# Optimization experiments

Hardware: AMD Instinct MI355X
Metric: run time of the kernel (lower is better)

Reference implementation:

```python
import jax, jax.numpy as jnp
import numpy as np

EMB = 64   # embedding_dim
OUT = 64   # out_channels (== EMB so conv layers stack)
EF = 16    # num_edge_features
L = 2      # num_layers
NC, NT = 5000, 10000
E, EL = 50000, 20000


def setup_inputs():
    key = jax.random.key(0)
    it = iter(jax.random.split(key, 40))
    def nrm(shape, s=0.05):
        return jax.random.normal(next(it), shape, dtype=jnp.float32) * s
    def ri(n, hi):
        return jax.random.randint(next(it), (n,), 0, hi, dtype=jnp.int32)
    return dict(
        x_c=jnp.arange(NC, dtype=jnp.int32),
        x_t=jnp.arange(NT, dtype=jnp.int32),
        edge_src_ct=ri(E, NC), edge_dst_ct=ri(E, NT),
        edge_src_tc=ri(E, NT), edge_dst_tc=ri(E, NC),
        edge_label_src=ri(EL, NC), edge_label_dst=ri(EL, NT),
        edge_attr_ct=nrm((E, EF), 1.0),
        edge_attr_tc=nrm((E, EF), 1.0),
        edge_label_attr=nrm((EL, EF), 1.0),
        emb_c=nrm((NC, EMB), 1.0), emb_t=nrm((NT, EMB), 1.0),
        ntl_c_w=nrm((EMB, EMB)), ntl_c_b=nrm((EMB,)),
        ntl_t_w=nrm((EMB, EMB)), ntl_t_b=nrm((EMB,)),
        conv_mlp1_w=nrm((L, 2, EF, OUT)), conv_mlp1_b=nrm((L, 2, OUT)),
        conv_mlp2_w=nrm((L, 2, OUT, EMB * OUT)), conv_mlp2_b=nrm((L, 2, EMB * OUT)),
        conv_root_w=nrm((L, 2, EMB, OUT)), conv_root_b=nrm((L, 2, OUT)),
        ph_w0=nrm((2 * EMB + EF, 64)), ph_b0=nrm((64,)),
        ph_w1=nrm((64, 64)), ph_b1=nrm((64,)),
        ph_w2=nrm((64, 1)), ph_b2=nrm((1,)),
    )


def _nnconv(h_src, h_dst, src, dst, eattr, m1w, m1b, m2w, m2b, rw, rb, n_dst):
    # edge-conditioned weight matrices: [E, EMB, OUT]
    W = (jax.nn.relu(eattr @ m1w + m1b) @ m2w + m2b).reshape(-1, EMB, OUT)
    msg = jnp.einsum('ei,eio->eo', h_src[src], W)        # gather + per-edge matmul
    agg = jax.ops.segment_max(msg, dst, num_segments=n_dst)
    agg = jnp.where(jnp.isneginf(agg), 0.0, agg)         # isolated nodes -> 0 (PyG semantics)
    return agg + h_dst @ rw + rb                          # root weight + bias


def reference(x_c, x_t, edge_src_ct, edge_dst_ct, edge_src_tc, edge_dst_tc,
              edge_label_src, edge_label_dst, edge_attr_ct, edge_attr_tc,
              edge_label_attr, emb_c, emb_t, ntl_c_w, ntl_c_b, ntl_t_w, ntl_t_b,
              conv_mlp1_w, conv_mlp1_b, conv_mlp2_w, conv_mlp2_b,
              conv_root_w, conv_root_b, ph_w0, ph_b0, ph_w1, ph_b1, ph_w2, ph_b2):
    h_c = emb_c[x_c] @ ntl_c_w + ntl_c_b
    h_t = emb_t[x_t] @ ntl_t_w + ntl_t_b
    for l in range(L):
        new_t = _nnconv(h_c, h_t, edge_src_ct, edge_dst_ct, edge_attr_ct,
                        conv_mlp1_w[l, 0], conv_mlp1_b[l, 0], conv_mlp2_w[l, 0],
                        conv_mlp2_b[l, 0], conv_root_w[l, 0], conv_root_b[l, 0], NT)
        new_c = _nnconv(h_t, h_c, edge_src_tc, edge_dst_tc, edge_attr_tc,
                        conv_mlp1_w[l, 1], conv_mlp1_b[l, 1], conv_mlp2_w[l, 1],
                        conv_mlp2_b[l, 1], conv_root_w[l, 1], conv_root_b[l, 1], NC)
        h_c, h_t = jax.nn.relu(new_c), jax.nn.relu(new_t)
    z = jnp.concatenate([h_c[edge_label_src], h_t[edge_label_dst], edge_label_attr], axis=-1)
    z = jax.nn.relu(z @ ph_w0 + ph_b0)
    z = jax.nn.relu(z @ ph_w1 + ph_b1)
    logits = z @ ph_w2 + ph_b2
    preds = jax.nn.sigmoid(logits).squeeze()
    return preds, logits
```

## Files before the change

kernel.cpp:

```cpp
#include <hip/hip_runtime.h>
#include <hip/hip_bf16.h>
#include <math.h>

#define NCN   5000
#define NTN   10000
#define NEDGE 50000
#define NLBL  20000
#define EPB   448
#define EBLK  112
#define ESLOT 50176
#define MT    7

typedef _Float16 f16x8 __attribute__((ext_vector_type(8)));
typedef _Float16 f16x4 __attribute__((ext_vector_type(4)));
typedef float    f32x4 __attribute__((ext_vector_type(4)));

#define HSTRIDE 456
#define NSLICE  130
#define ZSTR    72

__device__ __forceinline__ void stage16(const _Float16* g, _Float16* l) {
  __builtin_amdgcn_global_load_lds(
      (const __attribute__((address_space(1))) void*)g,
      (__attribute__((address_space(3))) void*)l, 16, 0, 0);
}

__global__ __launch_bounds__(256) void prep_B(
    const float* __restrict__ m2w, const float* __restrict__ m2b,
    _Float16* __restrict__ out)
{
  int p = blockIdx.x / NSLICE;
  int s = blockIdx.x % NSLICE;
  int t = threadIdx.x;
  int hi = t >> 6, col = t & 63;
  const float* w  = m2w + p * 64 * 4096;
  const float* bb = m2b + p * 4096;
  f16x8 v;
  #pragma unroll
  for (int j = 0; j < 8; ++j) {
    float x;
    if (s < 128) {
      int h = s >> 1, i = (s & 1) * 32 + hi * 8 + j;
      x = w[h * 4096 + i * 64 + col];
    } else {
      int i = (s - 128) * 32 + hi * 8 + j;
      x = bb[i * 64 + col];
    }
    v[j] = (_Float16)x;
  }
  *(f16x8*)(out + ((size_t)(p * NSLICE + s)) * 2048 + t * 8) = v;
}

__global__ __launch_bounds__(256) void prep_m1(
    const float* __restrict__ m1w, const float* __restrict__ m1b,
    _Float16* __restrict__ out)
{
  int p = blockIdx.x;
  int t = threadIdx.x;
  int hi = t >> 6, col = t & 63;
  f16x8 v;
  #pragma unroll
  for (int j = 0; j < 8; ++j) {
    int i = hi * 8 + j;
    float x = (i < 16) ? m1w[p * 1024 + i * 64 + col]
            : (i == 16) ? m1b[p * 64 + col] : 0.0f;
    v[j] = (_Float16)x;
  }
  *(f16x8*)(out + (size_t)p * 2048 + t * 8) = v;
}

__global__ __launch_bounds__(256) void prep_headB(
    const float* __restrict__ w0, const float* __restrict__ b0,
    const float* __restrict__ w1, const float* __restrict__ b1,
    _Float16* __restrict__ out)
{
  int s = blockIdx.x;
  int t = threadIdx.x;
  int hi = t >> 6, col = t & 63;
  f16x8 v;
  #pragma unroll
  for (int j = 0; j < 8; ++j) {
    int k = hi * 8 + j;
    float x = 0.0f;
    if (s < 5) {
      int kr = s * 32 + k;
      x = (kr < 144) ? w0[kr * 64 + col] : (kr == 144 ? b0[col] : 0.0f);
    } else {
      int kr = (s - 5) * 32 + k;
      x = (kr < 64) ? w1[kr * 64 + col] : (kr == 64 ? b1[col] : 0.0f);
    }
    v[j] = (_Float16)x;
  }
  *(f16x8*)(out + (size_t)s * 2048 + t * 8) = v;
}

__global__ __launch_bounds__(256) void count_edges(
    const int* __restrict__ dT, const int* __restrict__ dC,
    int* __restrict__ cT, int* __restrict__ cC)
{
  int i = blockIdx.x * 256 + threadIdx.x;
  if (i < NEDGE) atomicAdd(&cT[dT[i]], 1);
  else { int j = i - NEDGE; if (j < NEDGE) atomicAdd(&cC[dC[j]], 1); }
}

struct ScanArgs { const int* c0; int* o0; int n0; const int* c1; int* o1; int n1; };

__global__ __launch_bounds__(1024) void scan2(ScanArgs a) {
  const int* c = blockIdx.x ? a.c1 : a.c0;
  int*       o = blockIdx.x ? a.o1 : a.o0;
  int        n = blockIdx.x ? a.n1 : a.n0;
  __shared__ int lds[1024];
  int t = threadIdx.x;
  int CH = (n + 1023) / 1024;
  int base = t * CH;
  int s = 0;
  for (int i = 0; i < CH; ++i) { int idx = base + i; if (idx < n) s += c[idx]; }
  lds[t] = s;
  __syncthreads();
  #pragma unroll
  for (int d = 1; d < 1024; d <<= 1) {
    int v = (t >= d) ? lds[t - d] : 0;
    __syncthreads();
    lds[t] += v;
    __syncthreads();
  }
  int run = lds[t] - s;
  for (int i = 0; i < CH; ++i) {
    int idx = base + i;
    if (idx < n) { o[idx] = run; run += c[idx]; }
  }
  if (t == 1023) o[n] = lds[1023];
}

__global__ __launch_bounds__(256) void scatter_edges(
    const int* __restrict__ dT, const int* __restrict__ dC,
    const int* __restrict__ oT, const int* __restrict__ oC,
    int* __restrict__ curT, int* __restrict__ curC,
    int* __restrict__ permT, int* __restrict__ permC)
{
  int i = blockIdx.x * 256 + threadIdx.x;
  if (i < NEDGE) {
    int d = dT[i];
    int p = atomicAdd(&curT[d], 1);
    permT[oT[d] + p] = i;
  } else {
    int j = i - NEDGE;
    if (j < NEDGE) {
      int d = dC[j];
      int p = atomicAdd(&curC[d], 1);
      permC[oC[d] + p] = j;
    }
  }
}

struct NtArgs {
  const float* emb0; const int* idx0; const float* w0; const float* b0; float* out0; int n0; int blk0;
  const float* emb1; const int* idx1; const float* w1; const float* b1; float* out1; int n1;
};

__global__ __launch_bounds__(256) void node_transform2(NtArgs a) {
  int bid = blockIdx.x;
  int dir = (bid >= a.blk0) ? 1 : 0;
  int lb  = bid - (dir ? a.blk0 : 0);
  const float* emb = dir ? a.emb1 : a.emb0;
  const int*   idx = dir ? a.idx1 : a.idx0;
  const float* w   = dir ? a.w1   : a.w0;
  const float* b   = dir ? a.b1   : a.b0;
  float*       out = dir ? a.out1 : a.out0;
  int          n   = dir ? a.n1   : a.n0;

  __shared__ float s_w[64 * 64];
  __shared__ float s_b[64];
  int tid = threadIdx.x;
  for (int i = tid; i < 4096; i += 256) s_w[i] = w[i];
  if (tid < 64) s_b[tid] = b[tid];
  __syncthreads();
  int wave = tid >> 6, lane = tid & 63;
  int node = lb * 4 + wave;
  if (node >= n) return;
  float v = emb[idx[node] * 64 + lane];
  float acc = s_b[lane];
  #pragma unroll 8
  for (int i = 0; i < 64; ++i)
    acc = fmaf(__shfl(v, i, 64), s_w[i * 64 + lane], acc);
  out[node * 64 + lane] = acc;
}

struct ConvArgs {
  const float* h_src0; const int* esrc0; const float* ea0;
  const int* perm0; const _Float16* B0; const _Float16* m10; float* msg0;
  const float* h_src1; const int* esrc1; const float* ea1;
  const int* perm1; const _Float16* B1; const _Float16* m11; float* msg1;
};

__global__ __launch_bounds__(256, 1) void conv_msg_mfma2(ConvArgs a) {
  __shared__ __align__(16) _Float16 s_B[2][4][2048];
  __shared__ __align__(16) _Float16 s_m1f[2048];
  __shared__ __align__(16) _Float16 s_hidT[64 * HSTRIDE];
  __shared__ int s_srcn[EPB];
  __shared__ int s_eidx[EPB];

  const int bid = blockIdx.x;
  const int dir = (bid >= EBLK) ? 1 : 0;
  const int eb  = bid - (dir ? EBLK : 0);

  const float*    h_src  = dir ? a.h_src1 : a.h_src0;
  const int*      esrc   = dir ? a.esrc1  : a.esrc0;
  const float*    eattr  = dir ? a.ea1    : a.ea0;
  const int*      eperm  = dir ? a.perm1  : a.perm0;
  const _Float16* Bready = dir ? a.B1     : a.B0;
  const _Float16* m1rdy  = dir ? a.m11    : a.m10;
  float*          msg    = dir ? a.msg1   : a.msg0;

  const int tid  = threadIdx.x;
  const int e0   = eb * EPB;
  const int w    = tid >> 6;
  const int lane = tid & 63;
  const int l15  = lane & 15;
  const int hi   = lane >> 4;
  const int wE   = w * (MT * 16);

  stage16(m1rdy + tid * 8, &s_m1f[tid * 8]);
  #pragma unroll
  for (int q = 0; q < 4; ++q)
    stage16(Bready + (size_t)q * 2048 + tid * 8, &s_B[0][q][tid * 8]);

  for (int i = tid; i < EPB; i += 256) {
    int e = eperm[e0 + i];
    s_eidx[i] = e;
    s_srcn[i] = esrc[e];
  }
  __syncthreads();

  f16x8 hv0[MT], hv1[MT];
  #pragma unroll
  for (int m = 0; m < MT; ++m) {
    int el = wE + m * 16 + l15;
    const float* src = h_src + (size_t)s_srcn[el] * 64;
    float4 a0 = *(const float4*)(src + hi * 8);
    float4 a1 = *(const float4*)(src + hi * 8 + 4);
    float4 b0 = *(const float4*)(src + 32 + hi * 8);
    float4 b1 = *(const float4*)(src + 32 + hi * 8 + 4);
    hv0[m] = (f16x8){(_Float16)a0.x,(_Float16)a0.y,(_Float16)a0.z,(_Float16)a0.w,
                     (_Float16)a1.x,(_Float16)a1.y,(_Float16)a1.z,(_Float16)a1.w};
    hv1[m] = (f16x8){(_Float16)b0.x,(_Float16)b0.y,(_Float16)b0.z,(_Float16)b0.w,
                     (_Float16)b1.x,(_Float16)b1.y,(_Float16)b1.z,(_Float16)b1.w};
  }

  {
    f16x8 ea[MT];
    #pragma unroll
    for (int m = 0; m < MT; ++m) {
      int li = wE + m * 16 + l15;
      int e  = s_eidx[li];
      f16x8 v = {};
      if (hi < 2) {
        float4 f0 = *(const float4*)(eattr + (size_t)e * 16 + hi * 8);
        float4 f1 = *(const float4*)(eattr + (size_t)e * 16 + hi * 8 + 4);
        v = (f16x8){(_Float16)f0.x,(_Float16)f0.y,(_Float16)f0.z,(_Float16)f0.w,
                    (_Float16)f1.x,(_Float16)f1.y,(_Float16)f1.z,(_Float16)f1.w};
      } else if (hi == 2) {
        v[0] = (_Float16)1.0f;
      }
      ea[m] = v;
    }
    #pragma unroll
    for (int n = 0; n < 4; ++n) {
      f16x8 bm = *(const f16x8*)&s_m1f[(hi * 64 + n * 16 + l15) * 8];
      #pragma unroll
      for (int m = 0; m < MT; ++m) {
        f32x4 hacc = {};
        hacc = __builtin_amdgcn_mfma_f32_16x16x32_f16(ea[m], bm, hacc, 0, 0, 0);
        int h  = n * 16 + l15;
        int e4 = wE + m * 16 + hi * 4;
        f16x4 hval;
        #pragma unroll
        for (int r = 0; r < 4; ++r) hval[r] = (_Float16)fmaxf(hacc[r], 0.0f);
        *(f16x4*)&s_hidT[h * HSTRIDE + e4] = hval;
      }
    }
  }

  f32x4 acc[MT][4] = {};

#define MFMA_SLICE(P_, SS, HV, HH)                                            \
  {                                                                           \
    f16x8 b0 = *(const f16x8*)&s_B[P_][SS][(hi * 64 +  0 + l15) * 8];         \
    f16x8 b1 = *(const f16x8*)&s_B[P_][SS][(hi * 64 + 16 + l15) * 8];         \
    f16x8 b2 = *(const f16x8*)&s_B[P_][SS][(hi * 64 + 32 + l15) * 8];         \
    f16x8 b3 = *(const f16x8*)&s_B[P_][SS][(hi * 64 + 48 + l15) * 8];         \
    _Pragma("unroll")                                                         \
    for (int m = 0; m < MT; ++m) {                                            \
      f16x8 av = (f16x8)(HV[m] * HH[m]);                                      \
      acc[m][0] = __builtin_amdgcn_mfma_f32_16x16x32_f16(av, b0, acc[m][0], 0, 0, 0); \
      acc[m][1] = __builtin_amdgcn_mfma_f32_16x16x32_f16(av, b1, acc[m][1], 0, 0, 0); \
      acc[m][2] = __builtin_amdgcn_mfma_f32_16x16x32_f16(av, b2, acc[m][2], 0, 0, 0); \
      acc[m][3] = __builtin_amdgcn_mfma_f32_16x16x32_f16(av, b3, acc[m][3], 0, 0, 0); \
    }                                                                         \
  }

#define BIAS_SLICE(P_, SS, HV)                                                \
  {                                                                           \
    f16x8 b0 = *(const f16x8*)&s_B[P_][SS][(hi * 64 +  0 + l15) * 8];         \
    f16x8 b1 = *(const f16x8*)&s_B[P_][SS][(hi * 64 + 16 + l15) * 8];         \
    f16x8 b2 = *(const f16x8*)&s_B[P_][SS][(hi * 64 + 32 + l15) * 8];         \
    f16x8 b3 = *(const f16x8*)&s_B[P_][SS][(hi * 64 + 48 + l15) * 8];         \
    _Pragma("unroll")                                                         \
    for (int m = 0; m < MT; ++m) {                                            \
      f16x8 av = HV[m];                                                       \
      acc[m][0] = __builtin_amdgcn_mfma_f32_16x16x32_f16(av, b0, acc[m][0], 0, 0, 0); \
      acc[m][1] = __builtin_amdgcn_mfma_f32_16x16x32_f16(av, b1, acc[m][1], 0, 0, 0); \
      acc[m][2] = __builtin_amdgcn_mfma_f32_16x16x32_f16(av, b2, acc[m][2], 0, 0, 0); \
      acc[m][3] = __builtin_amdgcn_mfma_f32_16x16x32_f16(av, b3, acc[m][3], 0, 0, 0); \
    }                                                                         \
  }

  for (int p = 0; p < 33; ++p) {
    const int P = p & 1;
    if (p < 31) {
      #pragma unroll
      for (int q = 0; q < 4; ++q)
        stage16(Bready + (size_t)(4 * p + 4 + q) * 2048 + tid * 8,
                &s_B[P ^ 1][q][tid * 8]);
    } else if (p == 31) {
      stage16(Bready + (size_t)128 * 2048 + tid * 8, &s_B[P ^ 1][0][tid * 8]);
      stage16(Bready + (size_t)129 * 2048 + tid * 8, &s_B[P ^ 1][1][tid * 8]);
    }
    if (p < 32) {
      _Float16 hA[MT], hB[MT];
      #pragma unroll
      for (int m = 0; m < MT; ++m)
        hA[m] = s_hidT[(2 * p) * HSTRIDE + wE + m * 16 + l15];
      #pragma unroll
      for (int m = 0; m < MT; ++m)
        hB[m] = s_hidT[(2 * p + 1) * HSTRIDE + wE + m * 16 + l15];
      MFMA_SLICE(P, 0, hv0, hA);
      MFMA_SLICE(P, 1, hv1, hA);
      MFMA_SLICE(P, 2, hv0, hB);
      MFMA_SLICE(P, 3, hv1, hB);
    } else {
      BIAS_SLICE(P, 0, hv0);
      BIAS_SLICE(P, 1, hv1);
    }
    asm volatile("s_waitcnt vmcnt(0)" ::: "memory");
    __builtin_amdgcn_s_barrier();
  }
#undef MFMA_SLICE
#undef BIAS_SLICE

  #pragma unroll
  for (int m = 0; m < MT; ++m) {
    #pragma unroll
    for (int r = 0; r < 4; ++r) {
      int sl = e0 + wE + m * 16 + hi * 4 + r;
      float* row = msg + (size_t)sl * 64;
      #pragma unroll
      for (int n = 0; n < 4; ++n)
        row[n * 16 + l15] = acc[m][n][r];
    }
  }
}

struct SegArgs {
  const float* msg0; const int* off0; const float* hold0; const float* rw0; const float* rb0;
  float* hnew0; int n0; int blk0;
  const float* msg1; const int* off1; const float* hold1; const float* rw1; const float* rb1;
  float* hnew1; int n1;
};

__global__ __launch_bounds__(256) void segfin2(SegArgs a) {
  int bid = blockIdx.x;
  int dir = (bid >= a.blk0) ? 1 : 0;
  int lb  = bid - (dir ? a.blk0 : 0);
  const float* msg  = dir ? a.msg1  : a.msg0;
  const int*   off  = dir ? a.off1  : a.off0;
  const float* hold = dir ? a.hold1 : a.hold0;
  const float* rw   = dir ? a.rw1   : a.rw0;
  const float* rb   = dir ? a.rb1   : a.rb0;
  float*       hnew = dir ? a.hnew1 : a.hnew0;
  int          n    = dir ? a.n1    : a.n0;

  __shared__ float s_w[64 * 64];
  __shared__ float s_b[64];
  int tid = threadIdx.x;
  for (int i = tid; i < 4096; i += 256) s_w[i] = rw[i];
  if (tid < 64) s_b[tid] = rb[tid];
  __syncthreads();
  int wave = tid >> 6, lane = tid & 63;
  int node = lb * 4 + wave;
  if (node >= n) return;

  int k0 = off[node], k1 = off[node + 1];
  float mx = -INFINITY;
  for (int k = k0; k < k1; ++k)
    mx = fmaxf(mx, msg[(size_t)k * 64 + lane]);
  if (k0 == k1) mx = 0.0f;

  float v = hold[node * 64 + lane];
  float acc = s_b[lane];
  #pragma unroll 8
  for (int i = 0; i < 64; ++i)
    acc = fmaf(__shfl(v, i, 64), s_w[i * 64 + lane], acc);
  hnew[node * 64 + lane] = fmaxf(mx + acc, 0.0f);
}

__global__ __launch_bounds__(256) void head_mfma(
    const float* __restrict__ h_c, const float* __restrict__ h_t,
    const int* __restrict__ lsrc, const int* __restrict__ ldst,
    const float* __restrict__ lattr,
    const _Float16* __restrict__ headB,
    const float* __restrict__ w2, const float* __restrict__ b2,
    float* __restrict__ preds, float* __restrict__ logits, int nL)
{
  __shared__ __align__(16) _Float16 s_W[8][2048];
  __shared__ __align__(16) _Float16 s_z[4][32][ZSTR];
  __shared__ float s_w2[64];

  const int tid = threadIdx.x;
  const int wv = tid >> 6, lane = tid & 63;
  const int l15 = lane & 15, hi = lane >> 4;

  #pragma unroll
  for (int s = 0; s < 8; ++s)
    stage16(headB + s * 2048 + tid * 8, &s_W[s][tid * 8]);
  if (tid < 64) s_w2[tid] = w2[tid];
  const float b2v = b2[0];

  const int e0 = blockIdx.x * 128 + wv * 32;

  f16x8 ac[2][2], at[2][2], aa[2];
  #pragma unroll
  for (int m = 0; m < 2; ++m) {
    int e = e0 + m * 16 + l15;
    int ee = (e < nL) ? e : 0;
    const float* pc = h_c + (size_t)lsrc[ee] * 64;
    const float* pt = h_t + (size_t)ldst[ee] * 64;
    #pragma unroll
    for (int half = 0; half < 2; ++half) {
      float4 c0 = *(const float4*)(pc + half * 32 + hi * 8);
      float4 c1 = *(const float4*)(pc + half * 32 + hi * 8 + 4);
      float4 t0 = *(const float4*)(pt + half * 32 + hi * 8);
      float4 t1 = *(const float4*)(pt + half * 32 + hi * 8 + 4);
      ac[m][half] = (f16x8){(_Float16)c0.x,(_Float16)c0.y,(_Float16)c0.z,(_Float16)c0.w,
                            (_Float16)c1.x,(_Float16)c1.y,(_Float16)c1.z,(_Float16)c1.w};
      at[m][half] = (f16x8){(_Float16)t0.x,(_Float16)t0.y,(_Float16)t0.z,(_Float16)t0.w,
                            (_Float16)t1.x,(_Float16)t1.y,(_Float16)t1.z,(_Float16)t1.w};
    }
    f16x8 v = {};
    if (hi < 2) {
      float4 f0 = *(const float4*)(lattr + (size_t)ee * 16 + hi * 8);
      float4 f1 = *(const float4*)(lattr + (size_t)ee * 16 + hi * 8 + 4);
      v = (f16x8){(_Float16)f0.x,(_Float16)f0.y,(_Float16)f0.z,(_Float16)f0.w,
                  (_Float16)f1.x,(_Float16)f1.y,(_Float16)f1.z,(_Float16)f1.w};
    } else if (hi == 2) {
      v[0] = (_Float16)1.0f;
    }
    aa[m] = v;
  }

  __syncthreads();

  f32x4 acc1[2][4] = {};
  #pragma unroll
  for (int s = 0; s < 5; ++s) {
    f16x8 bfr[4];
    #pragma unroll
    for (int nn = 0; nn < 4; ++nn)
      bfr[nn] = *(const f16x8*)&s_W[s][(hi * 64 + nn * 16 + l15) * 8];
    #pragma unroll
    for (int m = 0; m < 2; ++m) {
      f16x8 a = (s == 0) ? ac[m][0] : (s == 1) ? ac[m][1]
              : (s == 2) ? at[m][0] : (s == 3) ? at[m][1] : aa[m];
      #pragma unroll
      for (int nn = 0; nn < 4; ++nn)
        acc1[m][nn] = __builtin_amdgcn_mfma_f32_16x16x32_f16(a, bfr[nn], acc1[m][nn], 0, 0, 0);
    }
  }

  #pragma unroll
  for (int m = 0; m < 2; ++m)
    #pragma unroll
    for (int nn = 0; nn < 4; ++nn)
      #pragma unroll
      for (int r = 0; r < 4; ++r)
        s_z[wv][m * 16 + hi * 4 + r][nn * 16 + l15] =
            (_Float16)fmaxf(acc1[m][nn][r], 0.0f);

  f16x8 abias = {};
  if (hi == 0) abias[0] = (_Float16)1.0f;
  f32x4 acc2[2][4] = {};
  #pragma unroll
  for (int s = 0; s < 3; ++s) {
    f16x8 bfr[4];
    #pragma unroll
    for (int nn = 0; nn < 4; ++nn)
      bfr[nn] = *(const f16x8*)&s_W[5 + s][(hi * 64 + nn * 16 + l15) * 8];
    #pragma unroll
    for (int m = 0; m < 2; ++m) {
      f16x8 a = (s < 2) ? *(const f16x8*)&s_z[wv][m * 16 + l15][s * 32 + hi * 8] : abias;
      #pragma unroll
      for (int nn = 0; nn < 4; ++nn)
        acc2[m][nn] = __builtin_amdgcn_mfma_f32_16x16x32_f16(a, bfr[nn], acc2[m][nn], 0, 0, 0);
    }
  }

  #pragma unroll
  for (int m = 0; m < 2; ++m) {
    float part[4];
    #pragma unroll
    for (int r = 0; r < 4; ++r) {
      float p = 0.0f;
      #pragma unroll
      for (int nn = 0; nn < 4; ++nn)
        p = fmaf(fmaxf(acc2[m][nn][r], 0.0f), s_w2[nn * 16 + l15], p);
      part[r] = p;
    }
    #pragma unroll
    for (int off = 1; off < 16; off <<= 1) {
      #pragma unroll
      for (int r = 0; r < 4; ++r)
        part[r] += __shfl_xor(part[r], off, 64);
    }
    if (l15 == 0) {
      #pragma unroll
      for (int r = 0; r < 4; ++r) {
        int e = e0 + m * 16 + hi * 4 + r;
        if (e < nL) {
          float lg = part[r] + b2v;
          logits[e] = lg;
          preds[e]  = 1.0f / (1.0f + expf(-lg));
        }
      }
    }
  }
}

extern "C" void kernel_launch(void* const* d_in, const int* in_sizes, int n_in,
                              void* d_out, int out_size, void* d_ws, size_t ws_size,
                              hipStream_t stream) {
  const int*   x_c      = (const int*)  d_in[0];
  const int*   x_t      = (const int*)  d_in[1];
  const int*   esrc_ct  = (const int*)  d_in[2];
  const int*   edst_ct  = (const int*)  d_in[3];
  const int*   esrc_tc  = (const int*)  d_in[4];
  const int*   edst_tc  = (const int*)  d_in[5];
  const int*   lbl_src  = (const int*)  d_in[6];
  const int*   lbl_dst  = (const int*)  d_in[7];
  const float* eattr_ct = (const float*)d_in[8];
  const float* eattr_tc = (const float*)d_in[9];
  const float* lbl_attr = (const float*)d_in[10];
  const float* emb_c    = (const float*)d_in[11];
  const float* emb_t    = (const float*)d_in[12];
  const float* ntl_c_w  = (const float*)d_in[13];
  const float* ntl_c_b  = (const float*)d_in[14];
  const float* ntl_t_w  = (const float*)d_in[15];
  const float* ntl_t_b  = (const float*)d_in[16];
  const float* m1w      = (const float*)d_in[17];
  const float* m1b      = (const float*)d_in[18];
  const float* m2w      = (const float*)d_in[19];
  const float* m2b      = (const float*)d_in[20];
  const float* rw       = (const float*)d_in[21];
  const float* rb       = (const float*)d_in[22];
  const float* ph_w0    = (const float*)d_in[23];
  const float* ph_b0    = (const float*)d_in[24];
  const float* ph_w1    = (const float*)d_in[25];
  const float* ph_b1    = (const float*)d_in[26];
  const float* ph_w2    = (const float*)d_in[27];
  const float* ph_b2    = (const float*)d_in[28];

  float* out = (float*)d_out;

  float* ws = (float*)d_ws;
  float* h_c0 = ws;
  float* h_c1 = h_c0 + NCN * 64;
  float* h_t0 = h_c1 + NCN * 64;
  float* h_t1 = h_t0 + NTN * 64;
  float* msgT = h_t1 + NTN * 64;
  float* msgC = msgT + (size_t)ESLOT * 64;
  _Float16* Bready  = (_Float16*)(msgC + (size_t)ESLOT * 64);
  _Float16* m1ready = Bready + 4 * NSLICE * 2048;
  _Float16* headBr  = m1ready + 4 * 2048;
  int* ip     = (int*)(headBr + 8 * 2048);
  int* offT   = ip;               ip += NTN + 1;
  int* offC   = ip;               ip += NCN + 1;
  int* cntT   = ip;               ip += NTN;
  int* cntC   = ip;               ip += NCN;
  int* curT   = ip;               ip += NTN;
  int* curC   = ip;               ip += NCN;
  int* permT  = ip;               ip += ESLOT;
  int* permC  = ip;               ip += ESLOT;
  size_t zero_bytes = (size_t)(2 * (NTN + NCN) + 2 * ESLOT) * sizeof(int);

  hipMemsetAsync(cntT, 0, zero_bytes, stream);
  count_edges<<<(2 * NEDGE + 255) / 256, 256, 0, stream>>>(edst_ct, edst_tc, cntT, cntC);
  {
    ScanArgs sa; sa.c0 = cntT; sa.o0 = offT; sa.n0 = NTN;
    sa.c1 = cntC; sa.o1 = offC; sa.n1 = NCN;
    scan2<<<2, 1024, 0, stream>>>(sa);
  }
  scatter_edges<<<(2 * NEDGE + 255) / 256, 256, 0, stream>>>(
      edst_ct, edst_tc, offT, offC, curT, curC, permT, permC);

  prep_B    <<<4 * NSLICE, 256, 0, stream>>>(m2w, m2b, Bready);
  prep_m1   <<<4, 256, 0, stream>>>(m1w, m1b, m1ready);
  prep_headB<<<8, 256, 0, stream>>>(ph_w0, ph_b0, ph_w1, ph_b1, headBr);

  {
    NtArgs na;
    na.emb0 = emb_c; na.idx0 = x_c; na.w0 = ntl_c_w; na.b0 = ntl_c_b; na.out0 = h_c0; na.n0 = NCN;
    na.blk0 = (NCN + 3) / 4;
    na.emb1 = emb_t; na.idx1 = x_t; na.w1 = ntl_t_w; na.b1 = ntl_t_b; na.out1 = h_t0; na.n1 = NTN;
    node_transform2<<<(NCN + 3) / 4 + (NTN + 3) / 4, 256, 0, stream>>>(na);
  }

  float* hc_cur = h_c0; float* hc_nxt = h_c1;
  float* ht_cur = h_t0; float* ht_nxt = h_t1;

  for (int l = 0; l < 2; ++l) {
    int p0 = l * 2 + 0;
    int p1 = l * 2 + 1;
    {
      ConvArgs ca;
      ca.h_src0 = hc_cur; ca.esrc0 = esrc_ct; ca.ea0 = eattr_ct; ca.perm0 = permT;
      ca.B0 = Bready + (size_t)p0 * NSLICE * 2048; ca.m10 = m1ready + (size_t)p0 * 2048;
      ca.msg0 = msgT;
      ca.h_src1 = ht_cur; ca.esrc1 = esrc_tc; ca.ea1 = eattr_tc; ca.perm1 = permC;
      ca.B1 = Bready + (size_t)p1 * NSLICE * 2048; ca.m11 = m1ready + (size_t)p1 * 2048;
      ca.msg1 = msgC;
      conv_msg_mfma2<<<2 * EBLK, 256, 0, stream>>>(ca);
    }
    {
      SegArgs sg;
      sg.msg0 = msgT; sg.off0 = offT; sg.hold0 = ht_cur;
      sg.rw0 = rw + p0 * 4096; sg.rb0 = rb + p0 * 64; sg.hnew0 = ht_nxt;
      sg.n0 = NTN; sg.blk0 = (NTN + 3) / 4;
      sg.msg1 = msgC; sg.off1 = offC; sg.hold1 = hc_cur;
      sg.rw1 = rw + p1 * 4096; sg.rb1 = rb + p1 * 64; sg.hnew1 = hc_nxt;
      sg.n1 = NCN;
      segfin2<<<(NTN + 3) / 4 + (NCN + 3) / 4, 256, 0, stream>>>(sg);
    }
    float* t;
    t = hc_cur; hc_cur = hc_nxt; hc_nxt = t;
    t = ht_cur; ht_cur = ht_nxt; ht_nxt = t;
  }

  head_mfma<<<(NLBL + 127) / 128, 256, 0, stream>>>(
      hc_cur, ht_cur, lbl_src, lbl_dst, lbl_attr,
      headBr, ph_w2, ph_b2,
      out, out + NLBL, NLBL);
}
```

Before: 254.9 us.

## Shrink conv blocks to 128 edges, merge prep kernels, batch nodes per wave

The edge-message kernel now runs 128 edges per block with 2 waves instead of 448 edges with 4 waves. That gives 392 blocks per direction to fill the GPU better. The m1 staging buffer now reuses an s_B slot, with an extra barrier, and each stage is split into two 16-byte loads per thread. The three weight-prep kernels are merged into one launch. The node transform and segment-finalize kernels now process 8 nodes per wave, which cuts the number of blocks that each reload the 64x64 weight into LDS. Smaller conv tiles re-stream the full B matrix more times per edge.

```diff
diff --git a/kernel.cpp b/kernel.cpp
--- a/kernel.cpp
+++ b/kernel.cpp
@@ -6,16 +6,16 @@
 #define NTN   10000
 #define NEDGE 50000
 #define NLBL  20000
-#define EPB   448
-#define EBLK  112
+#define EPB   128
+#define EBLK  392
 #define ESLOT 50176
-#define MT    7
+#define MT    4
 
 typedef _Float16 f16x8 __attribute__((ext_vector_type(8)));
 typedef _Float16 f16x4 __attribute__((ext_vector_type(4)));
 typedef float    f32x4 __attribute__((ext_vector_type(4)));
 
-#define HSTRIDE 456
+#define HSTRIDE 136
 #define NSLICE  130
 #define ZSTR    72
 
@@ -25,73 +25,62 @@
       (__attribute__((address_space(3))) void*)l, 16, 0, 0);
 }
 
-__global__ __launch_bounds__(256) void prep_B(
-    const float* __restrict__ m2w, const float* __restrict__ m2b,
-    _Float16* __restrict__ out)
-{
-  int p = blockIdx.x / NSLICE;
-  int s = blockIdx.x % NSLICE;
-  int t = threadIdx.x;
-  int hi = t >> 6, col = t & 63;
-  const float* w  = m2w + p * 64 * 4096;
-  const float* bb = m2b + p * 4096;
-  f16x8 v;
-  #pragma unroll
-  for (int j = 0; j < 8; ++j) {
-    float x;
-    if (s < 128) {
-      int h = s >> 1, i = (s & 1) * 32 + hi * 8 + j;
-      x = w[h * 4096 + i * 64 + col];
-    } else {
-      int i = (s - 128) * 32 + hi * 8 + j;
-      x = bb[i * 64 + col];
-    }
-    v[j] = (_Float16)x;
-  }
-  *(f16x8*)(out + ((size_t)(p * NSLICE + s)) * 2048 + t * 8) = v;
-}
-
-__global__ __launch_bounds__(256) void prep_m1(
-    const float* __restrict__ m1w, const float* __restrict__ m1b,
-    _Float16* __restrict__ out)
-{
-  int p = blockIdx.x;
+struct PrepArgs {
+  const float* m2w; const float* m2b; _Float16* outB;
+  const float* m1w; const float* m1b; _Float16* outM1;
+  const float* w0; const float* b0; const float* w1; const float* b1;
+  _Float16* outHead;
+};
+
+__global__ __launch_bounds__(256) void prep_all(PrepArgs a) {
+  int bid = blockIdx.x;
   int t = threadIdx.x;
   int hi = t >> 6, col = t & 63;
   f16x8 v;
-  #pragma unroll
-  for (int j = 0; j < 8; ++j) {
-    int i = hi * 8 + j;
-    float x = (i < 16) ? m1w[p * 1024 + i * 64 + col]
-            : (i == 16) ? m1b[p * 64 + col] : 0.0f;
-    v[j] = (_Float16)x;
-  }
-  *(f16x8*)(out + (size_t)p * 2048 + t * 8) = v;
-}
-
-__global__ __launch_bounds__(256) void prep_headB(
-    const float* __restrict__ w0, const float* __restrict__ b0,
-    const float* __restrict__ w1, const float* __restrict__ b1,
-    _Float16* __restrict__ out)
-{
-  int s = blockIdx.x;
-  int t = threadIdx.x;
-  int hi = t >> 6, col = t & 63;
-  f16x8 v;
-  #pragma unroll
-  for (int j = 0; j < 8; ++j) {
-    int k = hi * 8 + j;
-    float x = 0.0f;
-    if (s < 5) {
-      int kr = s * 32 + k;
-      x = (kr < 144) ? w0[kr * 64 + col] : (kr == 144 ? b0[col] : 0.0f);
-    } else {
-      int kr = (s - 5) * 32 + k;
-      x = (kr < 64) ? w1[kr * 64 + col] : (kr == 64 ? b1[col] : 0.0f);
-    }
-    v[j] = (_Float16)x;
-  }
-  *(f16x8*)(out + (size_t)s * 2048 + t * 8) = v;
+  if (bid < 4 * NSLICE) {
+    int p = bid / NSLICE, s = bid % NSLICE;
+    const float* w  = a.m2w + p * 64 * 4096;
+    const float* bb = a.m2b + p * 4096;
+    #pragma unroll
+    for (int j = 0; j < 8; ++j) {
+      float x;
+      if (s < 128) {
+        int h = s >> 1, i = (s & 1) * 32 + hi * 8 + j;
+        x = w[h * 4096 + i * 64 + col];
+      } else {
+        int i = (s - 128) * 32 + hi * 8 + j;
+        x = bb[i * 64 + col];
+      }
+      v[j] = (_Float16)x;
+    }
+    *(f16x8*)(a.outB + ((size_t)(p * NSLICE + s)) * 2048 + t * 8) = v;
+  } else if (bid < 4 * NSLICE + 4) {
+    int p = bid - 4 * NSLICE;
+    #pragma unroll
+    for (int j = 0; j < 8; ++j) {
+      int i = hi * 8 + j;
+      float x = (i < 16) ? a.m1w[p * 1024 + i * 64 + col]
+              : (i == 16) ? a.m1b[p * 64 + col] : 0.0f;
+      v[j] = (_Float16)x;
+    }
+    *(f16x8*)(a.outM1 + (size_t)p * 2048 + t * 8) = v;
+  } else {
+    int s = bid - (4 * NSLICE + 4);
+    #pragma unroll
+    for (int j = 0; j < 8; ++j) {
+      int k = hi * 8 + j;
+      float x = 0.0f;
+      if (s < 5) {
+        int kr = s * 32 + k;
+        x = (kr < 144) ? a.w0[kr * 64 + col] : (kr == 144 ? a.b0[col] : 0.0f);
+      } else {
+        int kr = (s - 5) * 32 + k;
+        x = (kr < 64) ? a.w1[kr * 64 + col] : (kr == 64 ? a.b1[col] : 0.0f);
+      }
+      v[j] = (_Float16)x;
+    }
+    *(f16x8*)(a.outHead + (size_t)s * 2048 + t * 8) = v;
+  }
 }
 
 __global__ __launch_bounds__(256) void count_edges(
@@ -176,14 +165,17 @@
   if (tid < 64) s_b[tid] = b[tid];
   __syncthreads();
   int wave = tid >> 6, lane = tid & 63;
-  int node = lb * 4 + wave;
-  if (node >= n) return;
-  float v = emb[idx[node] * 64 + lane];
-  float acc = s_b[lane];
-  #pragma unroll 8
-  for (int i = 0; i < 64; ++i)
-    acc = fmaf(__shfl(v, i, 64), s_w[i * 64 + lane], acc);
-  out[node * 64 + lane] = acc;
+  #pragma unroll
+  for (int it = 0; it < 8; ++it) {
+    int node = lb * 32 + wave * 8 + it;
+    if (node >= n) continue;
+    float v = emb[idx[node] * 64 + lane];
+    float acc = s_b[lane];
+    #pragma unroll 8
+    for (int i = 0; i < 64; ++i)
+      acc = fmaf(__shfl(v, i, 64), s_w[i * 64 + lane], acc);
+    out[node * 64 + lane] = acc;
+  }
 }
 
 struct ConvArgs {
@@ -193,9 +185,8 @@
   const int* perm1; const _Float16* B1; const _Float16* m11; float* msg1;
 };
 
-__global__ __launch_bounds__(256, 1) void conv_msg_mfma2(ConvArgs a) {
+__global__ __launch_bounds__(128) void conv_msg_mfma2(ConvArgs a) {
   __shared__ __align__(16) _Float16 s_B[2][4][2048];
-  __shared__ __align__(16) _Float16 s_m1f[2048];
   __shared__ __align__(16) _Float16 s_hidT[64 * HSTRIDE];
   __shared__ int s_srcn[EPB];
   __shared__ int s_eidx[EPB];
@@ -218,17 +209,20 @@
   const int lane = tid & 63;
   const int l15  = lane & 15;
   const int hi   = lane >> 4;
-  const int wE   = w * (MT * 16);
-
-  stage16(m1rdy + tid * 8, &s_m1f[tid * 8]);
-  #pragma unroll
-  for (int q = 0; q < 4; ++q)
-    stage16(Bready + (size_t)q * 2048 + tid * 8, &s_B[0][q][tid * 8]);
-
-  for (int i = tid; i < EPB; i += 256) {
-    int e = eperm[e0 + i];
-    s_eidx[i] = e;
-    s_srcn[i] = esrc[e];
+  const int wE   = w * 64;
+
+  stage16(m1rdy + tid * 8,        &s_B[1][0][tid * 8]);
+  stage16(m1rdy + 1024 + tid * 8, &s_B[1][0][1024 + tid * 8]);
+  #pragma unroll
+  for (int q = 0; q < 4; ++q) {
+    stage16(Bready + (size_t)q * 2048 + tid * 8,        &s_B[0][q][tid * 8]);
+    stage16(Bready + (size_t)q * 2048 + 1024 + tid * 8, &s_B[0][q][1024 + tid * 8]);
+  }
+
+  {
+    int e = eperm[e0 + tid];
+    s_eidx[tid] = e;
+    s_srcn[tid] = esrc[e];
   }
   __syncthreads();
 
@@ -266,7 +260,7 @@
     }
     #pragma unroll
     for (int n = 0; n < 4; ++n) {
-      f16x8 bm = *(const f16x8*)&s_m1f[(hi * 64 + n * 16 + l15) * 8];
+      f16x8 bm = *(const f16x8*)&s_B[1][0][(hi * 64 + n * 16 + l15) * 8];
       #pragma unroll
       for (int m = 0; m < MT; ++m) {
         f32x4 hacc = {};
@@ -280,6 +274,7 @@
       }
     }
   }
+  __syncthreads();
 
   f32x4 acc[MT][4] = {};
 
@@ -319,12 +314,20 @@
     const int P = p & 1;
     if (p < 31) {
       #pragma unroll
-      for (int q = 0; q < 4; ++q)
+      for (int q = 0; q < 4; ++q) {
         stage16(Bready + (size_t)(4 * p + 4 + q) * 2048 + tid * 8,
                 &s_B[P ^ 1][q][tid * 8]);
+        stage16(Bready + (size_t)(4 * p + 4 + q) * 2048 + 1024 + tid * 8,
+                &s_B[P ^ 1][q][1024 + tid * 8]);
+      }
     } else if (p == 31) {
-      stage16(Bready + (size_t)128 * 2048 + tid * 8, &s_B[P ^ 1][0][tid * 8]);
-      stage16(Bready + (size_t)129 * 2048 + tid * 8, &s_B[P ^ 1][1][tid * 8]);
+      #pragma unroll
+      for (int q = 0; q < 2; ++q) {
+        stage16(Bready + (size_t)(128 + q) * 2048 + tid * 8,
+                &s_B[P ^ 1][q][tid * 8]);
+        stage16(Bready + (size_t)(128 + q) * 2048 + 1024 + tid * 8,
+                &s_B[P ^ 1][q][1024 + tid * 8]);
+      }
     }
     if (p < 32) {
       _Float16 hA[MT], hB[MT];
@@ -387,21 +390,24 @@
   if (tid < 64) s_b[tid] = rb[tid];
   __syncthreads();
   int wave = tid >> 6, lane = tid & 63;
-  int node = lb * 4 + wave;
-  if (node >= n) return;
-
-  int k0 = off[node], k1 = off[node + 1];
-  float mx = -INFINITY;
-  for (int k = k0; k < k1; ++k)
-    mx = fmaxf(mx, msg[(size_t)k * 64 + lane]);
-  if (k0 == k1) mx = 0.0f;
-
-  float v = hold[node * 64 + lane];
-  float acc = s_b[lane];
-  #pragma unroll 8
-  for (int i = 0; i < 64; ++i)
-    acc = fmaf(__shfl(v, i, 64), s_w[i * 64 + lane], acc);
-  hnew[node * 64 + lane] = fmaxf(mx + acc, 0.0f);
+  #pragma unroll
+  for (int it = 0; it < 8; ++it) {
+    int node = lb * 32 + wave * 8 + it;
+    if (node >= n) continue;
+
+    int k0 = off[node], k1 = off[node + 1];
+    float mx = -INFINITY;
+    for (int k = k0; k < k1; ++k)
+      mx = fmaxf(mx, msg[(size_t)k * 64 + lane]);
+    if (k0 == k1) mx = 0.0f;
+
+    float v = hold[node * 64 + lane];
+    float acc = s_b[lane];
+    #pragma unroll 8
+    for (int i = 0; i < 64; ++i)
+      acc = fmaf(__shfl(v, i, 64), s_w[i * 64 + lane], acc);
+    hnew[node * 64 + lane] = fmaxf(mx + acc, 0.0f);
+  }
 }
 
 __global__ __launch_bounds__(256) void head_mfma(
@@ -601,16 +607,21 @@
   scatter_edges<<<(2 * NEDGE + 255) / 256, 256, 0, stream>>>(
       edst_ct, edst_tc, offT, offC, curT, curC, permT, permC);
 
-  prep_B    <<<4 * NSLICE, 256, 0, stream>>>(m2w, m2b, Bready);
-  prep_m1   <<<4, 256, 0, stream>>>(m1w, m1b, m1ready);
-  prep_headB<<<8, 256, 0, stream>>>(ph_w0, ph_b0, ph_w1, ph_b1, headBr);
+  {
+    PrepArgs pa;
+    pa.m2w = m2w; pa.m2b = m2b; pa.outB = Bready;
+    pa.m1w = m1w; pa.m1b = m1b; pa.outM1 = m1ready;
+    pa.w0 = ph_w0; pa.b0 = ph_b0; pa.w1 = ph_w1; pa.b1 = ph_b1;
+    pa.outHead = headBr;
+    prep_all<<<4 * NSLICE + 4 + 8, 256, 0, stream>>>(pa);
+  }
 
   {
     NtArgs na;
     na.emb0 = emb_c; na.idx0 = x_c; na.w0 = ntl_c_w; na.b0 = ntl_c_b; na.out0 = h_c0; na.n0 = NCN;
-    na.blk0 = (NCN + 3) / 4;
+    na.blk0 = (NCN + 31) / 32;
     na.emb1 = emb_t; na.idx1 = x_t; na.w1 = ntl_t_w; na.b1 = ntl_t_b; na.out1 = h_t0; na.n1 = NTN;
-    node_transform2<<<(NCN + 3) / 4 + (NTN + 3) / 4, 256, 0, stream>>>(na);
+    node_transform2<<<(NCN + 31) / 32 + (NTN + 31) / 32, 256, 0, stream>>>(na);
   }
 
   float* hc_cur = h_c0; float* hc_nxt = h_c1;
@@ -627,17 +638,17 @@
       ca.h_src1 = ht_cur; ca.esrc1 = esrc_tc; ca.ea1 = eattr_tc; ca.perm1 = permC;
       ca.B1 = Bready + (size_t)p1 * NSLICE * 2048; ca.m11 = m1ready + (size_t)p1 * 2048;
       ca.msg1 = msgC;
-      conv_msg_mfma2<<<2 * EBLK, 256, 0, stream>>>(ca);
+      conv_msg_mfma2<<<2 * EBLK, 128, 0, stream>>>(ca);
     }
     {
       SegArgs sg;
       sg.msg0 = msgT; sg.off0 = offT; sg.hold0 = ht_cur;
       sg.rw0 = rw + p0 * 4096; sg.rb0 = rb + p0 * 64; sg.hnew0 = ht_nxt;
-      sg.n0 = NTN; sg.blk0 = (NTN + 3) / 4;
+      sg.n0 = NTN; sg.blk0 = (NTN + 31) / 32;
       sg.msg1 = msgC; sg.off1 = offC; sg.hold1 = hc_cur;
       sg.rw1 = rw + p1 * 4096; sg.rb1 = rb + p1 * 64; sg.hnew1 = hc_nxt;
       sg.n1 = NCN;
-      segfin2<<<(NTN + 3) / 4 + (NCN + 3) / 4, 256, 0, stream>>>(sg);
+      segfin2<<<(NTN + 31) / 32 + (NCN + 31) / 32, 256, 0, stream>>>(sg);
     }
     float* t;
     t = hc_cur; hc_cur = hc_nxt; hc_nxt = t;
```

New measurement: 318.0 us. +24.8%, slower.
